# Kernel tuning notes

Measured on AMD Instinct MI355X. Metric: run time of the kernel, lower is better.

Reference implementation:

```python
import jax, jax.numpy as jnp
import numpy as np

D_MODEL = 1024
NUM_HEADS = 16
HEAD_DIM = D_MODEL // NUM_HEADS


def setup_inputs() -> dict:
    key = jax.random.key(0)
    k1, k2, k3 = jax.random.split(key, 3)
    x = jax.random.normal(k1, (2, 2048, D_MODEL), dtype=jnp.float32)
    a_qkv = (6.0 / (D_MODEL + 3 * D_MODEL)) ** 0.5
    w_qkv = jax.random.uniform(k2, (3 * D_MODEL, D_MODEL), jnp.float32, -a_qkv, a_qkv)
    a_p = (6.0 / (D_MODEL + D_MODEL)) ** 0.5
    w_proj = jax.random.uniform(k3, (D_MODEL, D_MODEL), jnp.float32, -a_p, a_p)
    return {"in_features": x, "w_qkv": w_qkv, "w_proj": w_proj}


def reference(in_features, w_qkv, w_proj):
    B, S, _ = in_features.shape
    qkv = jnp.einsum('bsi,ji->bsj', in_features, w_qkv)  # [B,S,3*D]
    # split (3, head, d_k) from last dim, -> [3, B, H, S, d_k]
    qkv = qkv.reshape(B, S, 3, NUM_HEADS, HEAD_DIM)
    qkv = jnp.transpose(qkv, (2, 0, 3, 1, 4))
    q, k, v = qkv[0], qkv[1], qkv[2]
    q = q * (HEAD_DIM ** -0.5)
    weight = jnp.einsum('bhqd,bhkd->bhqk', q, k)  # [B,H,S,S]
    causal = jnp.tril(jnp.ones((S, S), dtype=bool))
    weight = jnp.where(causal, weight, -jnp.inf)
    score = jax.nn.softmax(weight, axis=-1)
    attn = jnp.einsum('bhqk,bhkd->bhqd', score, v)
    attn = jnp.transpose(attn, (0, 2, 1, 3)).reshape(B, S, D_MODEL)
    return jnp.einsum('bsi,ji->bsj', attn, w_proj)
```

## Files before the change

kernel.cpp:

```cpp
#include <hip/hip_runtime.h>

#define S_LEN 2048
#define DM 1024
#define NH 16
#define HD 64
#define QKV_LD 3072

using f32x4 = __attribute__((ext_vector_type(4))) float;
using s16x8 = __attribute__((ext_vector_type(8))) short;

__device__ __forceinline__ unsigned short f2bf(float f) {
  union { float f; unsigned u; } v; v.f = f;
  unsigned r = v.u + 0x7fffu + ((v.u >> 16) & 1u);
  return (unsigned short)(r >> 16);
}

__device__ __forceinline__ float bf2f(unsigned short u) {
  union { unsigned u; float f; } v; v.u = ((unsigned)u) << 16;
  return v.f;
}

__device__ __forceinline__ void gload_lds16(const void* g, void* l) {
  __builtin_amdgcn_global_load_lds(
      (const __attribute__((address_space(1))) void*)g,
      (__attribute__((address_space(3))) void*)l, 16, 0, 0);
}

__device__ __forceinline__ int xcd_swz(int bid, int nwg) {
  const int cpx = nwg >> 3;
  return (bid & 7) * cpx + (bid >> 3);
}

__global__ __launch_bounds__(256) void cvt_f32_bf16(const float* __restrict__ in,
                                                    unsigned short* __restrict__ out,
                                                    int n) {
  int i = (blockIdx.x * 256 + threadIdx.x) * 8;
  if (i >= n) return;
  float4 a = *(const float4*)(in + i);
  float4 b = *(const float4*)(in + i + 4);
  s16x8 o;
  o[0] = f2bf(a.x); o[1] = f2bf(a.y); o[2] = f2bf(a.z); o[3] = f2bf(a.w);
  o[4] = f2bf(b.x); o[5] = f2bf(b.y); o[6] = f2bf(b.z); o[7] = f2bf(b.w);
  *(s16x8*)(out + i) = o;
}

template <int BN, bool OUT_F32>
__global__ __launch_bounds__(256, 3) void gemm_bt(const unsigned short* __restrict__ A,
                                                  const unsigned short* __restrict__ W,
                                                  void* __restrict__ Cout,
                                                  int M, int N, int K, int nbn) {
  constexpr int FN = BN / 32;
  constexpr int ROUNDS = (128 + BN) / 32;
  __shared__ unsigned short As[128 * 64];
  __shared__ unsigned short Bs[BN * 64];
  const int bid = xcd_swz(blockIdx.x, gridDim.x);
  const int bm = bid / nbn, bn = bid % nbn;
  const int tid = threadIdx.x;
  const int w = tid >> 6, lane = tid & 63;
  const int wr = w >> 1, wc = w & 1;
  const int lr = lane & 15, lk = lane >> 4;
  const int m0 = bm * 128, n0 = bn * BN;
  f32x4 acc[4][FN] = {};

  for (int k0 = 0; k0 < K; k0 += 64) {
#pragma unroll
    for (int j = 0; j < ROUNDS; ++j) {
      const int base = j * 4096 + w * 1024;
      const int boff = base + lane * 16;
      const int row = boff >> 7;
      const int col = (boff >> 1) & 63;
      if (j < 4)
        gload_lds16(A + (size_t)(m0 + row) * K + k0 + col, (char*)As + base);
      else
        gload_lds16(W + (size_t)(n0 + row - 128) * K + k0 + col,
                    (char*)Bs + base - 16384);
    }
    __syncthreads();
#pragma unroll
    for (int kk = 0; kk < 2; ++kk) {
      s16x8 af[4], bfr[FN];
#pragma unroll
      for (int m = 0; m < 4; ++m)
        af[m] = *(const s16x8*)((const char*)As + (wr * 64 + m * 16 + lr) * 128 + kk * 64 + lk * 16);
#pragma unroll
      for (int n = 0; n < FN; ++n)
        bfr[n] = *(const s16x8*)((const char*)Bs + (wc * (FN * 16) + n * 16 + lr) * 128 + kk * 64 + lk * 16);
#pragma unroll
      for (int m = 0; m < 4; ++m)
#pragma unroll
        for (int n = 0; n < FN; ++n)
          acc[m][n] = __builtin_amdgcn_mfma_f32_16x16x32_bf16(af[m], bfr[n], acc[m][n], 0, 0, 0);
    }
    __syncthreads();
  }
#pragma unroll
  for (int m = 0; m < 4; ++m)
#pragma unroll
    for (int n = 0; n < FN; ++n)
#pragma unroll
      for (int r = 0; r < 4; ++r) {
        const int row = m0 + wr * 64 + m * 16 + lk * 4 + r;
        const int col = n0 + wc * (FN * 16) + n * 16 + lr;
        if (OUT_F32)
          ((float*)Cout)[(size_t)row * N + col] = acc[m][n][r];
        else
          ((unsigned short*)Cout)[(size_t)row * N + col] = f2bf(acc[m][n][r]);
      }
}

__global__ __launch_bounds__(256) void vtrans(const unsigned short* __restrict__ qkv,
                                              unsigned short* __restrict__ vt) {
  __shared__ unsigned short T[64][65];
  const int blk = blockIdx.x;
  const int st = blk & 31, bh = blk >> 5;
  const int h = bh & 15, b = bh >> 4;
  const int s0 = st * 64;
  const int tid = threadIdx.x;
#pragma unroll
  for (int i = 0; i < 2; ++i) {
    const int idx = tid + i * 256;
    const int sy = idx >> 3, tx = idx & 7;
    s16x8 v = *(const s16x8*)(qkv + (size_t)(b * S_LEN + s0 + sy) * QKV_LD + 2 * DM + h * HD + tx * 8);
#pragma unroll
    for (int j = 0; j < 8; ++j) T[tx * 8 + j][sy] = v[j];
  }
  __syncthreads();
#pragma unroll
  for (int i = 0; i < 2; ++i) {
    const int idx = tid + i * 256;
    const int d = idx >> 3, tx = idx & 7;
    s16x8 v;
#pragma unroll
    for (int j = 0; j < 8; ++j) v[j] = T[d][tx * 8 + j];
    *(s16x8*)(vt + (size_t)bh * (HD * S_LEN) + (size_t)d * S_LEN + s0 + tx * 8) = v;
  }
}

__global__ __launch_bounds__(256, 3) void attn_fwd(const unsigned short* __restrict__ qkv,
                                                   const unsigned short* __restrict__ vt,
                                                   unsigned short* __restrict__ aout) {
  __shared__ unsigned short Ks[2][64 * 64];
  __shared__ unsigned short Vs[2][64 * 64];
  __shared__ unsigned short Pbuf[4][16][72];
  const int bid = blockIdx.x;
  const int qt = 31 - (bid >> 5);
  const int bh = bid & 31;
  const int h = bh & 15, b = bh >> 4;
  const int tid = threadIdx.x, w = tid >> 6, lane = tid & 63;
  const int lr = lane & 15, lk = lane >> 4;
  const int qb = qt * 64 + w * 16;
  const size_t rowbase = (size_t)b * S_LEN;
  const unsigned short* kbase = qkv + rowbase * QKV_LD + DM + h * HD;
  const unsigned short* vbase = vt + (size_t)bh * (HD * S_LEN);

  const int r8 = lane >> 3, c8 = lane & 7;
  const int celem = ((c8 ^ r8) << 3);
  const int swz = (lr & 7) << 3;

  s16x8 qf[2];
#pragma unroll
  for (int dk = 0; dk < 2; ++dk) {
    s16x8 q = *(const s16x8*)(qkv + (rowbase + qb + lr) * QKV_LD + h * HD + dk * 32 + lk * 8);
#pragma unroll
    for (int j = 0; j < 8; ++j)
      q[j] = (short)f2bf(bf2f((unsigned short)q[j]) * 0.18033688011112042f);
    qf[dk] = q;
  }

  f32x4 oacc[4] = {};
  float mr = -1e30f, ls = 0.f;

  auto stage = [&](int t, int c) {
    const int k0 = t * 64;
#pragma unroll
    for (int jj = 0; jj < 4; ++jj) {
      const int j = w * 4 + jj;
      if (j < 8)
        gload_lds16(kbase + (size_t)(k0 + j * 8 + r8) * QKV_LD + celem,
                    (char*)Ks[c] + j * 1024);
      else
        gload_lds16(vbase + (size_t)((j - 8) * 8 + r8) * S_LEN + k0 + celem,
                    (char*)Vs[c] + (j - 8) * 1024);
    }
  };

  stage(0, 0);
  __syncthreads();
  int c = 0;

  for (int t = 0; t <= qt; ++t) {
    if (t < qt) stage(t + 1, c ^ 1);

    const bool dtile = (t == qt);
    f32x4 sf[4];
    __builtin_amdgcn_s_setprio(1);
#pragma unroll
    for (int n = 0; n < 4; ++n) {
      if (!dtile || n <= w) {
        s16x8 kf0 = *(const s16x8*)(Ks[c] + (n * 16 + lr) * 64 + ((lk * 8) ^ swz));
        s16x8 kf1 = *(const s16x8*)(Ks[c] + (n * 16 + lr) * 64 + ((32 + lk * 8) ^ swz));
        f32x4 s = {};
        s = __builtin_amdgcn_mfma_f32_16x16x32_bf16(kf0, qf[0], s, 0, 0, 0);
        s = __builtin_amdgcn_mfma_f32_16x16x32_bf16(kf1, qf[1], s, 0, 0, 0);
        sf[n] = s;
      } else {
#pragma unroll
        for (int r = 0; r < 4; ++r) sf[n][r] = -1e30f;
      }
    }
    __builtin_amdgcn_s_setprio(0);
    if (dtile) {
#pragma unroll
      for (int r = 0; r < 4; ++r)
        if (lk * 4 + r > lr) sf[w][r] = -1e30f;
    }
    float pm = sf[0][0];
#pragma unroll
    for (int n = 0; n < 4; ++n)
#pragma unroll
      for (int r = 0; r < 4; ++r) pm = fmaxf(pm, sf[n][r]);
    pm = fmaxf(pm, __shfl_xor(pm, 16));
    pm = fmaxf(pm, __shfl_xor(pm, 32));
    if (__any(pm > mr + 8.f)) {
      const float mn = fmaxf(mr, pm);
      const float al = __builtin_amdgcn_exp2f(mr - mn);
      mr = mn;
      ls *= al;
#pragma unroll
      for (int r = 0; r < 4; ++r) {
        const float alq = __shfl(al, lk * 4 + r);
#pragma unroll
        for (int n = 0; n < 4; ++n) oacc[n][r] *= alq;
      }
    }
    float rs = 0.f;
#pragma unroll
    for (int n = 0; n < 4; ++n)
#pragma unroll
      for (int r = 0; r < 4; ++r) {
        const float p = __builtin_amdgcn_exp2f(sf[n][r] - mr);
        sf[n][r] = p;
        rs += p;
      }
    rs += __shfl_xor(rs, 16);
    rs += __shfl_xor(rs, 32);
    ls += rs;
#pragma unroll
    for (int n = 0; n < 4; ++n) {
      union { float f; unsigned u; } c0, c1, c2, c3;
      c0.f = sf[n][0]; c1.f = sf[n][1]; c2.f = sf[n][2]; c3.f = sf[n][3];
      uint2 pk;
      pk.x = ((c0.u + 0x8000u) >> 16) | (((c1.u + 0x8000u) >> 16) << 16);
      pk.y = ((c2.u + 0x8000u) >> 16) | (((c3.u + 0x8000u) >> 16) << 16);
      *(uint2*)&Pbuf[w][lr][n * 16 + lk * 4] = pk;
    }
    __builtin_amdgcn_s_setprio(1);
#pragma unroll
    for (int kk = 0; kk < 2; ++kk) {
      s16x8 pf = *(const s16x8*)&Pbuf[w][lr][kk * 32 + lk * 8];
#pragma unroll
      for (int n = 0; n < 4; ++n) {
        s16x8 vf = *(const s16x8*)(Vs[c] + (n * 16 + lr) * 64 + ((kk * 32 + lk * 8) ^ swz));
        oacc[n] = __builtin_amdgcn_mfma_f32_16x16x32_bf16(pf, vf, oacc[n], 0, 0, 0);
      }
    }
    __builtin_amdgcn_s_setprio(0);
    __syncthreads();
    c ^= 1;
  }

  const float rl = __builtin_amdgcn_rcpf(ls);
#pragma unroll
  for (int r = 0; r < 4; ++r) {
    const float rlq = __shfl(rl, lk * 4 + r);
#pragma unroll
    for (int n = 0; n < 4; ++n)
      aout[(rowbase + qb + lk * 4 + r) * DM + h * HD + n * 16 + lr] = f2bf(oacc[n][r] * rlq);
  }
}

extern "C" void kernel_launch(void* const* d_in, const int* in_sizes, int n_in,
                              void* d_out, int out_size, void* d_ws, size_t ws_size,
                              hipStream_t stream) {
  const float* x = (const float*)d_in[0];
  const float* wqkv = (const float*)d_in[1];
  const float* wproj = (const float*)d_in[2];
  float* out = (float*)d_out;

  char* ws = (char*)d_ws;
  unsigned short* xb = (unsigned short*)ws;
  unsigned short* wqkvb = (unsigned short*)(ws + (8u << 20));
  unsigned short* wprojb = (unsigned short*)(ws + (14u << 20));
  unsigned short* vtb = (unsigned short*)ws;
  unsigned short* qkvb = (unsigned short*)(ws + (16u << 20));
  unsigned short* attnb = (unsigned short*)(ws + (40u << 20));

  cvt_f32_bf16<<<2048, 256, 0, stream>>>(x, xb, 4096 * 1024);
  cvt_f32_bf16<<<1536, 256, 0, stream>>>(wqkv, wqkvb, 3072 * 1024);

  gemm_bt<128, false><<<32 * 24, 256, 0, stream>>>(xb, wqkvb, qkvb, 4096, 3072, 1024, 24);
  vtrans<<<1024, 256, 0, stream>>>(qkvb, vtb);
  attn_fwd<<<1024, 256, 0, stream>>>(qkvb, vtb, attnb);
  cvt_f32_bf16<<<512, 256, 0, stream>>>(wproj, wprojb, 1024 * 1024);
  gemm_bt<64, true><<<32 * 16, 256, 0, stream>>>(attnb, wprojb, out, 4096, 1024, 1024, 16);
}
```

Before: 182.4 us.

## Split QKV output into separate Q/K/V buffers and merge conversion kernels

The QKV GEMM epilogue now writes Q, K and V into three separate row-major [B*S,1024] buffers instead of one interleaved 3072-wide buffer. Attention and the V-transpose kernel read with a 1024 stride, which makes K tile loads denser. The three fp32-to-bf16 conversion launches are folded into one kernel that picks its source by thread index, removing two launches. The trade is a small per-thread branch in the conversion and a buffer select in the GEMM epilogue.

After: 178.4 us. 2.2% less time.

```diff
diff --git a/kernel.cpp b/kernel.cpp
--- a/kernel.cpp
+++ b/kernel.cpp
@@ -4,7 +4,6 @@
 #define DM 1024
 #define NH 16
 #define HD 64
-#define QKV_LD 3072
 
 using f32x4 = __attribute__((ext_vector_type(4))) float;
 using s16x8 = __attribute__((ext_vector_type(8))) short;
@@ -31,23 +30,34 @@
   return (bid & 7) * cpx + (bid >> 3);
 }
 
-__global__ __launch_bounds__(256) void cvt_f32_bf16(const float* __restrict__ in,
-                                                    unsigned short* __restrict__ out,
-                                                    int n) {
-  int i = (blockIdx.x * 256 + threadIdx.x) * 8;
-  if (i >= n) return;
-  float4 a = *(const float4*)(in + i);
-  float4 b = *(const float4*)(in + i + 4);
+__global__ __launch_bounds__(256) void cvt_all(const float* __restrict__ x,
+                                               const float* __restrict__ wqkv,
+                                               const float* __restrict__ wproj,
+                                               unsigned short* __restrict__ xb,
+                                               unsigned short* __restrict__ wqkvb,
+                                               unsigned short* __restrict__ wprojb) {
+  int it = blockIdx.x * 256 + threadIdx.x;
+  const float* src;
+  unsigned short* dst;
+  int off;
+  if (it < 524288)      { src = x;     dst = xb;     off = it; }
+  else if (it < 917504) { src = wqkv;  dst = wqkvb;  off = it - 524288; }
+  else                  { src = wproj; dst = wprojb; off = it - 917504; }
+  const int i = off * 8;
+  float4 a = *(const float4*)(src + i);
+  float4 b = *(const float4*)(src + i + 4);
   s16x8 o;
   o[0] = f2bf(a.x); o[1] = f2bf(a.y); o[2] = f2bf(a.z); o[3] = f2bf(a.w);
   o[4] = f2bf(b.x); o[5] = f2bf(b.y); o[6] = f2bf(b.z); o[7] = f2bf(b.w);
-  *(s16x8*)(out + i) = o;
+  *(s16x8*)(dst + i) = o;
 }
 
 template <int BN, bool OUT_F32>
 __global__ __launch_bounds__(256, 3) void gemm_bt(const unsigned short* __restrict__ A,
                                                   const unsigned short* __restrict__ W,
-                                                  void* __restrict__ Cout,
+                                                  void* __restrict__ C0,
+                                                  void* __restrict__ C1,
+                                                  void* __restrict__ C2,
                                                   int M, int N, int K, int nbn) {
   constexpr int FN = BN / 32;
   constexpr int ROUNDS = (128 + BN) / 32;
@@ -93,6 +103,9 @@
     }
     __syncthreads();
   }
+  const int sel = n0 >> 10;
+  void* Cs = (sel == 0) ? C0 : (sel == 1) ? C1 : C2;
+  const int nb0 = n0 & 1023;
 #pragma unroll
   for (int m = 0; m < 4; ++m)
 #pragma unroll
@@ -100,15 +113,15 @@
 #pragma unroll
       for (int r = 0; r < 4; ++r) {
         const int row = m0 + wr * 64 + m * 16 + lk * 4 + r;
-        const int col = n0 + wc * (FN * 16) + n * 16 + lr;
+        const int col = nb0 + wc * (FN * 16) + n * 16 + lr;
         if (OUT_F32)
-          ((float*)Cout)[(size_t)row * N + col] = acc[m][n][r];
+          ((float*)Cs)[(size_t)row * 1024 + col] = acc[m][n][r];
         else
-          ((unsigned short*)Cout)[(size_t)row * N + col] = f2bf(acc[m][n][r]);
-      }
-}
-
-__global__ __launch_bounds__(256) void vtrans(const unsigned short* __restrict__ qkv,
+          ((unsigned short*)Cs)[(size_t)row * 1024 + col] = f2bf(acc[m][n][r]);
+      }
+}
+
+__global__ __launch_bounds__(256) void vtrans(const unsigned short* __restrict__ vraw,
                                               unsigned short* __restrict__ vt) {
   __shared__ unsigned short T[64][65];
   const int blk = blockIdx.x;
@@ -120,7 +133,7 @@
   for (int i = 0; i < 2; ++i) {
     const int idx = tid + i * 256;
     const int sy = idx >> 3, tx = idx & 7;
-    s16x8 v = *(const s16x8*)(qkv + (size_t)(b * S_LEN + s0 + sy) * QKV_LD + 2 * DM + h * HD + tx * 8);
+    s16x8 v = *(const s16x8*)(vraw + (size_t)(b * S_LEN + s0 + sy) * DM + h * HD + tx * 8);
 #pragma unroll
     for (int j = 0; j < 8; ++j) T[tx * 8 + j][sy] = v[j];
   }
@@ -136,7 +149,8 @@
   }
 }
 
-__global__ __launch_bounds__(256, 3) void attn_fwd(const unsigned short* __restrict__ qkv,
+__global__ __launch_bounds__(256, 3) void attn_fwd(const unsigned short* __restrict__ qb_,
+                                                   const unsigned short* __restrict__ kb_,
                                                    const unsigned short* __restrict__ vt,
                                                    unsigned short* __restrict__ aout) {
   __shared__ unsigned short Ks[2][64 * 64];
@@ -150,7 +164,7 @@
   const int lr = lane & 15, lk = lane >> 4;
   const int qb = qt * 64 + w * 16;
   const size_t rowbase = (size_t)b * S_LEN;
-  const unsigned short* kbase = qkv + rowbase * QKV_LD + DM + h * HD;
+  const unsigned short* kbase = kb_ + rowbase * DM + h * HD;
   const unsigned short* vbase = vt + (size_t)bh * (HD * S_LEN);
 
   const int r8 = lane >> 3, c8 = lane & 7;
@@ -160,7 +174,7 @@
   s16x8 qf[2];
 #pragma unroll
   for (int dk = 0; dk < 2; ++dk) {
-    s16x8 q = *(const s16x8*)(qkv + (rowbase + qb + lr) * QKV_LD + h * HD + dk * 32 + lk * 8);
+    s16x8 q = *(const s16x8*)(qb_ + (rowbase + qb + lr) * DM + h * HD + dk * 32 + lk * 8);
 #pragma unroll
     for (int j = 0; j < 8; ++j)
       q[j] = (short)f2bf(bf2f((unsigned short)q[j]) * 0.18033688011112042f);
@@ -176,7 +190,7 @@
     for (int jj = 0; jj < 4; ++jj) {
       const int j = w * 4 + jj;
       if (j < 8)
-        gload_lds16(kbase + (size_t)(k0 + j * 8 + r8) * QKV_LD + celem,
+        gload_lds16(kbase + (size_t)(k0 + j * 8 + r8) * DM + celem,
                     (char*)Ks[c] + j * 1024);
       else
         gload_lds16(vbase + (size_t)((j - 8) * 8 + r8) * S_LEN + k0 + celem,
@@ -291,16 +305,17 @@
   unsigned short* xb = (unsigned short*)ws;
   unsigned short* wqkvb = (unsigned short*)(ws + (8u << 20));
   unsigned short* wprojb = (unsigned short*)(ws + (14u << 20));
+  unsigned short* qb = (unsigned short*)(ws + (16u << 20));
+  unsigned short* kb = (unsigned short*)(ws + (24u << 20));
+  unsigned short* vraw = (unsigned short*)(ws + (32u << 20));
   unsigned short* vtb = (unsigned short*)ws;
-  unsigned short* qkvb = (unsigned short*)(ws + (16u << 20));
   unsigned short* attnb = (unsigned short*)(ws + (40u << 20));
 
-  cvt_f32_bf16<<<2048, 256, 0, stream>>>(x, xb, 4096 * 1024);
-  cvt_f32_bf16<<<1536, 256, 0, stream>>>(wqkv, wqkvb, 3072 * 1024);
-
-  gemm_bt<128, false><<<32 * 24, 256, 0, stream>>>(xb, wqkvb, qkvb, 4096, 3072, 1024, 24);
-  vtrans<<<1024, 256, 0, stream>>>(qkvb, vtb);
-  attn_fwd<<<1024, 256, 0, stream>>>(qkvb, vtb, attnb);
-  cvt_f32_bf16<<<512, 256, 0, stream>>>(wproj, wprojb, 1024 * 1024);
-  gemm_bt<64, true><<<32 * 16, 256, 0, stream>>>(attnb, wprojb, out, 4096, 1024, 1024, 16);
-}
+  cvt_all<<<4096, 256, 0, stream>>>(x, wqkv, wproj, xb, wqkvb, wprojb);
+  gemm_bt<128, false><<<32 * 24, 256, 0, stream>>>(xb, wqkvb, qb, kb, vraw,
+                                                   4096, 3072, 1024, 24);
+  vtrans<<<1024, 256, 0, stream>>>(vraw, vtb);
+  attn_fwd<<<1024, 256, 0, stream>>>(qb, kb, vtb, attnb);
+  gemm_bt<64, true><<<32 * 16, 256, 0, stream>>>(attnb, wprojb, out, out, out,
+                                                 4096, 1024, 1024, 16);
+}
```
